# Kernel tuning notes

Measured on AMD Instinct MI355X. Metric: run time of the kernel, lower is better.

## Reference

```python
import jax, jax.numpy as jnp
import numpy as np

B, DX, DY, K, H = 131072, 256, 32, 4, 128
TIMESTEPS = 1000
LR, REG, SW = 0.1, 0.01, 1.0


def setup_inputs() -> dict:
    key = jax.random.key(0)
    ks = jax.random.split(key, 12)
    n = lambda k, shp, s=0.05: (jax.random.normal(k, shp) * s).astype(jnp.float32)
    return {
        "x": jax.random.normal(ks[0], (B, DX), jnp.float32),
        "t": jax.random.randint(ks[1], (B,), 0, K),
        "e_w1": n(ks[2], (DX + DY, H)), "e_b1": jnp.zeros((H,), jnp.float32),
        "e_w2": n(ks[3], (H, H)),       "e_b2": jnp.zeros((H,), jnp.float32),
        "e_w3": n(ks[4], (H, K)),       "e_b3": jnp.zeros((K,), jnp.float32),
        "s_xw": n(ks[5], (DX, H)),      "s_xb": jnp.zeros((H,), jnp.float32),
        "s_yw": n(ks[6], (DY, H)),      "s_yb": jnp.zeros((H,), jnp.float32),
        "s_temb": n(ks[7], (K, H)),
        "s_t1w": n(ks[8], (1, H)),      "s_t1b": jnp.zeros((H,), jnp.float32),
        "s_t2w": n(ks[9], (H, H)),      "s_t2b": jnp.zeros((H,), jnp.float32),
        "tr1w": n(ks[10], (4 * H, H)),  "tr1b": jnp.zeros((H,), jnp.float32),
        "tr2w": n(ks[11], (H, K)),      "tr2b": jnp.zeros((K,), jnp.float32),
        "steps": 20,
    }


def reference(x, t, e_w1, e_b1, e_w2, e_b2, e_w3, e_b3,
              s_xw, s_xb, s_yw, s_yb, s_temb, s_t1w, s_t1b, s_t2w, s_t2b,
              tr1w, tr1b, tr2w, tr2b, steps):
    tc = jnp.maximum(t, 0)                      # clamp_min(0)
    tci = tc[:, None]                           # [B,1] gather index
    valid = (t >= 0).astype(jnp.float32)[:, None]
    tau = jnp.maximum(tc.astype(jnp.float32) / TIMESTEPS, 1e-6)[:, None]  # [B,1]

    # y-independent precomputations (hoisted out of the loop)
    hx_e = x @ e_w1[:DX] + e_b1                 # energy first layer, x part [B,H]
    hx_s = x @ s_xw + s_xb                      # score x_proj [B,H]
    temb = s_temb[tc]                           # t embedding [B,H]
    th = jax.nn.silu(tau @ s_t1w + s_t1b) @ s_t2w + s_t2b  # time_fc [B,H]

    def total_fn(y):
        # EnergyNet: Linear-ReLU-Linear-ReLU-Linear on cat([x,y])
        h1 = jax.nn.relu(hx_e + y @ e_w1[DX:])
        e_all = jax.nn.relu(h1 @ e_w2 + e_b2) @ e_w3 + e_b3          # [B,K]
        e = jnp.take_along_axis(e_all, tci, axis=1)                  # [B,1]
        tot = e + REG * jnp.sum(y * y, axis=1, keepdims=True)
        # ScoreNet trunk on cat([x_proj, y_proj, t_embed, time_fc])
        hy = y @ s_yw + s_yb
        h = jnp.concatenate([hx_s, hy, temb, th], axis=-1)           # [B,4H]
        logits = jax.nn.silu(h @ tr1w + tr1b) @ tr2w + tr2b          # [B,K]
        ce = jax.nn.logsumexp(logits, axis=-1, keepdims=True) - jnp.take_along_axis(logits, tci, axis=1)
        return jnp.sum(tot + SW * ce * valid)

    grad_fn = jax.grad(total_fn)

    def step(carry, _):
        y, done = carry
        g = grad_fn(y)
        done = done | (jnp.sqrt(jnp.sum(g * g)) < 1e-3)  # torch: break before update
        y = jnp.where(done, y, y - LR * g)
        return (y, done), None

    y0 = jnp.zeros((x.shape[0], DY), jnp.float32)
    (y, _), _ = jax.lax.scan(step, (y0, jnp.array(False)), None, length=steps)
    return y
```

## Files before the change

### kernel.cpp

```cpp
#include <hip/hip_runtime.h>
#include <hip/hip_bf16.h>

#define DXc 256
#define DYc 32
#define Kc 4
#define Hc 128
#define LRf 0.1f
#define REGf 0.01f
#define TSTEPS 1000

typedef __attribute__((ext_vector_type(8))) short s8b;
typedef __attribute__((ext_vector_type(4))) float f32x4;

#define MFMA16(a, b, c) __builtin_amdgcn_mfma_f32_16x16x32_bf16((a), (b), (c), 0, 0, 0)

#define MFMA6(A0, A1, A2, B0, B1, B2, acc)      \
    do {                                        \
        acc = MFMA16((A0), (B0), acc);          \
        acc = MFMA16((A0), (B1), acc);          \
        acc = MFMA16((A1), (B0), acc);          \
        acc = MFMA16((A0), (B2), acc);          \
        acc = MFMA16((A1), (B1), acc);          \
        acc = MFMA16((A2), (B0), acc);          \
    } while (0)

__device__ __forceinline__ float hipart(float a) {
    return __uint_as_float(__float_as_uint(a) & 0xffff0000u);
}
__device__ __forceinline__ unsigned hi2(float a, float b) {
    return (__float_as_uint(a) >> 16) | (__float_as_uint(b) & 0xffff0000u);
}
__device__ __forceinline__ void wsplit(float x, unsigned short* __restrict__ h,
                                       unsigned short* __restrict__ l) {
    unsigned u = __float_as_uint(x);
    *h = (unsigned short)(u >> 16);
    float hf = __uint_as_float(u & 0xffff0000u);
    *l = (unsigned short)(__float_as_uint(x - hf) >> 16);
}
__device__ __forceinline__ void wsplit3(float x, unsigned short* __restrict__ p0,
                                        unsigned short* __restrict__ p1,
                                        unsigned short* __restrict__ p2) {
    unsigned u = __float_as_uint(x);
    *p0 = (unsigned short)(u >> 16);
    float r1 = x - __uint_as_float(u & 0xffff0000u);
    unsigned u1 = __float_as_uint(r1);
    *p1 = (unsigned short)(u1 >> 16);
    float r2 = r1 - __uint_as_float(u1 & 0xffff0000u);
    *p2 = (unsigned short)(__float_as_uint(r2) >> 16);
}
__device__ __forceinline__ void split3x8(const float* v, s8b& A0, s8b& A1, s8b& A2) {
    union { s8b s; unsigned u[4]; } P0, P1, P2;
    #pragma unroll
    for (int m = 0; m < 4; ++m) {
        float a = v[2 * m], b = v[2 * m + 1];
        unsigned ua = __float_as_uint(a), ub = __float_as_uint(b);
        P0.u[m] = (ua >> 16) | (ub & 0xffff0000u);
        float ra = a - __uint_as_float(ua & 0xffff0000u);
        float rb = b - __uint_as_float(ub & 0xffff0000u);
        unsigned ura = __float_as_uint(ra), urb = __float_as_uint(rb);
        P1.u[m] = (ura >> 16) | (urb & 0xffff0000u);
        float ra2 = ra - __uint_as_float(ura & 0xffff0000u);
        float rb2 = rb - __uint_as_float(urb & 0xffff0000u);
        P2.u[m] = (__float_as_uint(ra2) >> 16) | (__float_as_uint(rb2) & 0xffff0000u);
    }
    A0 = P0.s; A1 = P1.s; A2 = P2.s;
}
__device__ __forceinline__ void split3pack4(const float* v, uint2& Q0, uint2& Q1, uint2& Q2) {
    float r1[4], r2[4];
    #pragma unroll
    for (int i = 0; i < 4; ++i) {
        r1[i] = v[i] - hipart(v[i]);
        r2[i] = r1[i] - hipart(r1[i]);
    }
    Q0.x = hi2(v[0], v[1]);   Q0.y = hi2(v[2], v[3]);
    Q1.x = hi2(r1[0], r1[1]); Q1.y = hi2(r1[2], r1[3]);
    Q2.x = hi2(r2[0], r2[1]); Q2.y = hi2(r2[2], r2[3]);
}
__device__ __forceinline__ void split2pack4(const float* v, uint2& Q0, uint2& Q1) {
    Q0.x = hi2(v[0], v[1]); Q0.y = hi2(v[2], v[3]);
    float r0 = v[0] - hipart(v[0]), r1 = v[1] - hipart(v[1]);
    float r2 = v[2] - hipart(v[2]), r3 = v[3] - hipart(v[3]);
    Q1.x = hi2(r0, r1); Q1.y = hi2(r2, r3);
}

__global__ __launch_bounds__(256) void setup_kernel(
    const float* __restrict__ e_w1, const float* __restrict__ s_xw,
    const float* __restrict__ s_yw, const float* __restrict__ s_temb,
    const float* __restrict__ s_t1w, const float* __restrict__ s_t1b,
    const float* __restrict__ s_t2w, const float* __restrict__ s_t2b,
    const float* __restrict__ tr1w, const float* __restrict__ tr1b,
    const float* __restrict__ s_xb, const float* __restrict__ s_yb,
    const float* __restrict__ e_w2, float* __restrict__ d0,
    unsigned short* __restrict__ WcatTb0, unsigned short* __restrict__ WcatTb1,
    unsigned short* __restrict__ WcatTb2,
    unsigned short* __restrict__ W1Tb0, unsigned short* __restrict__ W1Tb1,
    unsigned short* __restrict__ W1Tb2,
    unsigned short* __restrict__ ew2Tb0, unsigned short* __restrict__ ew2Tb1,
    unsigned short* __restrict__ ew2Tb2,
    unsigned short* __restrict__ ew2bh, unsigned short* __restrict__ ew2bl,
    unsigned short* __restrict__ Wdybh, unsigned short* __restrict__ Wdybl)
{
    const int b = blockIdx.x;
    const int t = threadIdx.x;
    if (b < 64) {
        #pragma unroll
        for (int i = 0; i < 2; ++i) {
            int idx = t + 256 * i;
            int k = 4 * b + (idx >> 7);
            int c = idx & 127;
            float acc = 0.f;
            for (int h = 0; h < 128; ++h)
                acc += s_xw[k * 128 + h] * tr1w[h * 128 + c];
            wsplit3(acc, &WcatTb0[(128 + c) * 256 + k], &WcatTb1[(128 + c) * 256 + k],
                    &WcatTb2[(128 + c) * 256 + k]);
            float ev = e_w1[k * 128 + c];
            wsplit3(ev, &WcatTb0[c * 256 + k], &WcatTb1[c * 256 + k],
                    &WcatTb2[c * 256 + k]);
        }
    } else if (b == 64) {
        #pragma unroll
        for (int i = 0; i < 16; ++i) {
            int idx = t + 256 * i;
            int d = idx >> 7, c = idx & 127;
            float acc = 0.f;
            for (int h = 0; h < 128; ++h)
                acc += s_yw[d * 128 + h] * tr1w[(128 + h) * 128 + c];
            wsplit3(acc, &W1Tb0[(128 + c) * 32 + d], &W1Tb1[(128 + c) * 32 + d],
                    &W1Tb2[(128 + c) * 32 + d]);
            wsplit(acc, &Wdybh[d * 256 + c], &Wdybl[d * 256 + c]);
        }
    } else if (b == 65) {
        #pragma unroll
        for (int i = 0; i < 16; ++i) {
            int idx = t + 256 * i;
            int d = idx >> 7, c = idx & 127;
            float v = e_w1[(DXc + d) * 128 + c];
            wsplit3(v, &W1Tb0[c * 32 + d], &W1Tb1[c * 32 + d], &W1Tb2[c * 32 + d]);
            wsplit(v, &Wdybh[d * 256 + 128 + c], &Wdybl[d * 256 + 128 + c]);
        }
    } else if (b == 66) {
        #pragma unroll
        for (int i = 0; i < 64; ++i) {
            int idx = t + 256 * i;
            int h = idx >> 7, c = idx & 127;
            float v = e_w2[h * 128 + c];
            wsplit3(v, &ew2Tb0[c * 128 + h], &ew2Tb1[c * 128 + h],
                    &ew2Tb2[c * 128 + h]);
            wsplit(v, &ew2bh[h * 128 + c], &ew2bl[h * 128 + c]);
        }
    } else {
        __shared__ float thS[4][128];
        #pragma unroll
        for (int i = 0; i < 2; ++i) {
            int idx = t + 256 * i;
            int tt = idx >> 7, c = idx & 127;
            float tau = (float)tt / (float)TSTEPS;
            if (tau < 1e-6f) tau = 1e-6f;
            float acc = s_t2b[c];
            for (int h = 0; h < 128; ++h) {
                float aa = tau * s_t1w[h] + s_t1b[h];
                float s = 1.f / (1.f + expf(-aa));
                acc += aa * s * s_t2w[h * 128 + c];
            }
            thS[tt][c] = acc;
        }
        __syncthreads();
        #pragma unroll
        for (int i = 0; i < 2; ++i) {
            int idx = t + 256 * i;
            int tt = idx >> 7, c = idx & 127;
            float acc = tr1b[c];
            for (int h = 0; h < 128; ++h) {
                acc += s_temb[tt * 128 + h] * tr1w[(256 + h) * 128 + c];
                acc += thS[tt][h]           * tr1w[(384 + h) * 128 + c];
                acc += s_yb[h]              * tr1w[(128 + h) * 128 + c];
                acc += s_xb[h]              * tr1w[h * 128 + c];
            }
            d0[tt * 128 + c] = acc;
        }
    }
}

__global__ __launch_bounds__(256) void rowpre_kernel(
    const float* __restrict__ x, const int* __restrict__ tin,
    const unsigned short* __restrict__ WcatTb0,
    const unsigned short* __restrict__ WcatTb1,
    const unsigned short* __restrict__ WcatTb2,
    const float* __restrict__ e_b1, const float* __restrict__ d0,
    float* __restrict__ hxeP, float* __restrict__ cbP)
{
    __shared__ int tS[64];
    const int t = threadIdx.x;
    const int r0 = blockIdx.x * 64;
    const int w = t >> 6;
    const int l = t & 63;
    const int g = l >> 4, q = l & 15;
    if (t < 64) { int tv = tin[r0 + t]; tS[t] = tv > 0 ? tv : 0; }
    __syncthreads();

    for (int st = 0; st < 4; ++st) {
        const int smp = r0 + st * 16 + q;
        s8b Xb0[8], Xb1[8], Xb2[8];
        #pragma unroll
        for (int kc = 0; kc < 8; ++kc) {
            const float* xp = &x[(size_t)smp * 256 + kc * 32 + g * 8];
            float4 xa = *(const float4*)xp;
            float4 xb = *(const float4*)(xp + 4);
            float xv[8] = {xa.x, xa.y, xa.z, xa.w, xb.x, xb.y, xb.z, xb.w};
            split3x8(xv, Xb0[kc], Xb1[kc], Xb2[kc]);
        }
        #pragma unroll
        for (int ci = 0; ci < 4; ++ci) {
            const int colt = w * 4 + ci;
            f32x4 acc = {0.f, 0.f, 0.f, 0.f};
            #pragma unroll
            for (int kc = 0; kc < 8; ++kc) {
                const int wo = (colt * 16 + q) * 256 + kc * 32 + g * 8;
                s8b A0 = *(const s8b*)&WcatTb0[wo];
                s8b A1 = *(const s8b*)&WcatTb1[wo];
                s8b A2 = *(const s8b*)&WcatTb2[wo];
                MFMA6(A0, A1, A2, Xb0[kc], Xb1[kc], Xb2[kc], acc);
            }
            const int cb = colt * 16 + g * 4;
            if (colt < 8) {
                float4 bv = *(const float4*)&e_b1[cb];
                float4 o = {acc[0] + bv.x, acc[1] + bv.y, acc[2] + bv.z, acc[3] + bv.w};
                *(float4*)&hxeP[(size_t)smp * 128 + cb] = o;
            } else {
                const int cc = cb - 128;
                float4 dd = *(const float4*)&d0[tS[st * 16 + q] * 128 + cc];
                float4 o = {acc[0] + dd.x, acc[1] + dd.y, acc[2] + dd.z, acc[3] + dd.w};
                *(float4*)&cbP[(size_t)smp * 128 + cc] = o;
            }
        }
    }
}

__global__ __launch_bounds__(512) void iterate_kernel(
    const float* __restrict__ hxeP, const float* __restrict__ cbP,
    const unsigned short* __restrict__ W1Tb0, const unsigned short* __restrict__ W1Tb1,
    const unsigned short* __restrict__ W1Tb2,
    const unsigned short* __restrict__ ew2Tb0, const unsigned short* __restrict__ ew2Tb1,
    const unsigned short* __restrict__ ew2Tb2,
    const unsigned short* __restrict__ ew2bh, const unsigned short* __restrict__ ew2bl,
    const unsigned short* __restrict__ Wdybh, const unsigned short* __restrict__ Wdybl,
    const float* __restrict__ e_w3, const float* __restrict__ tr2w,
    const float* __restrict__ tr2b, const float* __restrict__ e_b2,
    const int* __restrict__ tin, const int* __restrict__ stepsPtr,
    float* __restrict__ yout)
{
    __shared__ __align__(16) unsigned short H1a[32 * 136];
    __shared__ __align__(16) unsigned short H1b[32 * 136];
    __shared__ __align__(16) unsigned short H1c[32 * 136];
    __shared__ __align__(16) unsigned short DAa[32 * 136], DAb[32 * 136];
    __shared__ __align__(16) float U[32 * 140];
    __shared__ __align__(16) float yS[32 * 36];
    __shared__ float ew3TS[512];
    __shared__ float eb2S[128];
    __shared__ float vSs[32];
    __shared__ int tcS[32];

    const int t = threadIdx.x;
    const int r0 = blockIdx.x * 32;
    const int w = t >> 6;
    const int l = t & 63;
    const int g = l >> 4;
    const int q = l & 15;
    const int row = t >> 4;
    const int p = t & 15;
    const int hA = 4 * p;
    const int hB = 64 + 4 * p;

    if (t < 32) {
        int tv = tin[r0 + t];
        tcS[t] = tv > 0 ? tv : 0;
        vSs[t] = (tv >= 0) ? 1.f : 0.f;
    }
    if (t < 128) eb2S[t] = e_b2[t];
    {
        const int k = t >> 7, c = t & 127;
        ew3TS[k * 128 + c] = e_w3[c * 4 + k];
    }
    for (int i = t; i < 32 * 36; i += 512) yS[i] = 0.f;

    float4 trw4[8];
    #pragma unroll
    for (int j = 0; j < 4; ++j) {
        trw4[j]     = *(const float4*)&tr2w[(hA + j) * 4];
        trw4[4 + j] = *(const float4*)&tr2w[(hB + j) * 4];
    }
    const float tb0 = tr2b[0], tb1 = tr2b[1], tb2 = tr2b[2], tb3 = tr2b[3];
    const int nsteps = stepsPtr[0];

    __syncthreads();

    for (int step = 0; step < nsteps; ++step) {
        {
            s8b WA0[2], WA1[2], WA2[2];
            #pragma unroll
            for (int ci = 0; ci < 2; ++ci) {
                const int arow = (2 * w + ci) * 16 + q;
                WA0[ci] = *(const s8b*)&W1Tb0[arow * 32 + g * 8];
                WA1[ci] = *(const s8b*)&W1Tb1[arow * 32 + g * 8];
                WA2[ci] = *(const s8b*)&W1Tb2[arow * 32 + g * 8];
            }
            #pragma unroll
            for (int ct = 0; ct < 2; ++ct) {
                float4 ya = *(const float4*)&yS[(ct * 16 + q) * 36 + g * 8];
                float4 yb = *(const float4*)&yS[(ct * 16 + q) * 36 + g * 8 + 4];
                float yv[8] = {ya.x, ya.y, ya.z, ya.w, yb.x, yb.y, yb.z, yb.w};
                s8b Y0, Y1, Y2;
                split3x8(yv, Y0, Y1, Y2);
                #pragma unroll
                for (int ci = 0; ci < 2; ++ci) {
                    const int colt = 2 * w + ci;
                    f32x4 acc = {0.f, 0.f, 0.f, 0.f};
                    MFMA6(WA0[ci], WA1[ci], WA2[ci], Y0, Y1, Y2, acc);
                    if (w < 4) {
                        const float4 vb = *(const float4*)
                            &hxeP[(size_t)(r0 + ct * 16 + q) * 128 + colt * 16 + g * 4];
                        float v[4];
                        v[0] = acc[0] + vb.x; v[1] = acc[1] + vb.y;
                        v[2] = acc[2] + vb.z; v[3] = acc[3] + vb.w;
                        #pragma unroll
                        for (int j = 0; j < 4; ++j) v[j] = v[j] > 0.f ? v[j] : 0.f;
                        uint2 Q0, Q1, Q2;
                        split3pack4(v, Q0, Q1, Q2);
                        const int off = (ct * 16 + q) * 136 + colt * 16 + g * 4;
                        *(uint2*)&H1a[off] = Q0;
                        *(uint2*)&H1b[off] = Q1;
                        *(uint2*)&H1c[off] = Q2;
                    } else {
                        const int cc = (colt - 8) * 16 + g * 4;
                        const float4 vb = *(const float4*)
                            &cbP[(size_t)(r0 + ct * 16 + q) * 128 + cc];
                        float4 o = {acc[0] + vb.x, acc[1] + vb.y,
                                    acc[2] + vb.z, acc[3] + vb.w};
                        *(float4*)&U[(ct * 16 + q) * 140 + cc] = o;
                    }
                }
            }
        }
        __syncthreads();

        {
            float aval[8], sval[8];
            float lg0 = 0.f, lg1 = 0.f, lg2 = 0.f, lg3 = 0.f;
            float4 v0 = *(const float4*)&U[row * 140 + hA];
            float4 v1 = *(const float4*)&U[row * 140 + hB];
            aval[0] = v0.x; aval[1] = v0.y; aval[2] = v0.z; aval[3] = v0.w;
            aval[4] = v1.x; aval[5] = v1.y; aval[6] = v1.z; aval[7] = v1.w;
            #pragma unroll
            for (int j = 0; j < 8; ++j) {
                float a = aval[j];
                float s = 1.f / (1.f + __expf(-a));
                sval[j] = s;
                float u = a * s;
                lg0 += u * trw4[j].x; lg1 += u * trw4[j].y;
                lg2 += u * trw4[j].z; lg3 += u * trw4[j].w;
            }
            #pragma unroll
            for (int m = 1; m < 16; m <<= 1) {
                lg0 += __shfl_xor(lg0, m);
                lg1 += __shfl_xor(lg1, m);
                lg2 += __shfl_xor(lg2, m);
                lg3 += __shfl_xor(lg3, m);
            }
            lg0 += tb0; lg1 += tb1; lg2 += tb2; lg3 += tb3;
            float mx = fmaxf(fmaxf(lg0, lg1), fmaxf(lg2, lg3));
            float e0 = __expf(lg0 - mx), e1 = __expf(lg1 - mx);
            float e2 = __expf(lg2 - mx), e3 = __expf(lg3 - mx);
            float inv = 1.f / (e0 + e1 + e2 + e3);
            int tcr = tcS[row];
            float vd = vSs[row];
            float dl0 = (e0 * inv - (tcr == 0 ? 1.f : 0.f)) * vd;
            float dl1 = (e1 * inv - (tcr == 1 ? 1.f : 0.f)) * vd;
            float dl2 = (e2 * inv - (tcr == 2 ? 1.f : 0.f)) * vd;
            float dl3 = (e3 * inv - (tcr == 3 ? 1.f : 0.f)) * vd;
            #pragma unroll
            for (int j = 0; j < 8; ++j) {
                float a = aval[j], s = sval[j];
                float du = dl0 * trw4[j].x + dl1 * trw4[j].y
                         + dl2 * trw4[j].z + dl3 * trw4[j].w;
                aval[j] = du * s * (1.f + a * (1.f - s));
            }
            float rl[8];
            #pragma unroll
            for (int j = 0; j < 8; ++j) rl[j] = aval[j] - hipart(aval[j]);
            uint2 QhA = {hi2(aval[0], aval[1]), hi2(aval[2], aval[3])};
            uint2 QhB = {hi2(aval[4], aval[5]), hi2(aval[6], aval[7])};
            uint2 QlA = {hi2(rl[0], rl[1]), hi2(rl[2], rl[3])};
            uint2 QlB = {hi2(rl[4], rl[5]), hi2(rl[6], rl[7])};
            *(uint2*)&DAa[row * 136 + hA] = QhA;
            *(uint2*)&DAa[row * 136 + hB] = QhB;
            *(uint2*)&DAb[row * 136 + hA] = QlA;
            *(uint2*)&DAb[row * 136 + hB] = QlB;
        }
        __syncthreads();

        {
            unsigned short* DZh = (unsigned short*)U;
            unsigned short* DZl = DZh + 32 * 136;
            const int hf = w & 1;
            const int ct0 = (w >> 1) * 2;
            f32x4 acc0 = {0.f, 0.f, 0.f, 0.f};
            f32x4 acc1 = {0.f, 0.f, 0.f, 0.f};
            #pragma unroll
            for (int kc = 0; kc < 4; ++kc) {
                const int boff = (hf * 16 + q) * 136 + kc * 32 + g * 8;
                s8b Ba = *(const s8b*)&H1a[boff];
                s8b Bb = *(const s8b*)&H1b[boff];
                s8b Bc = *(const s8b*)&H1c[boff];
                const int wo0 = ((ct0 + 0) * 16 + q) * 128 + kc * 32 + g * 8;
                const int wo1 = ((ct0 + 1) * 16 + q) * 128 + kc * 32 + g * 8;
                s8b A00 = *(const s8b*)&ew2Tb0[wo0];
                s8b A01 = *(const s8b*)&ew2Tb1[wo0];
                s8b A02 = *(const s8b*)&ew2Tb2[wo0];
                MFMA6(A00, A01, A02, Ba, Bb, Bc, acc0);
                s8b A10 = *(const s8b*)&ew2Tb0[wo1];
                s8b A11 = *(const s8b*)&ew2Tb1[wo1];
                s8b A12 = *(const s8b*)&ew2Tb2[wo1];
                MFMA6(A10, A11, A12, Ba, Bb, Bc, acc1);
            }
            const int smp = hf * 16 + q;
            const int tcr = tcS[smp];
            #pragma unroll
            for (int c2 = 0; c2 < 2; ++c2) {
                const f32x4& acc = c2 ? acc1 : acc0;
                const int cb = (ct0 + c2) * 16 + g * 4;
                const float4 eb = *(const float4*)&eb2S[cb];
                const float4 g4 = *(const float4*)&ew3TS[tcr * 128 + cb];
                float dz[4];
                dz[0] = (acc[0] + eb.x) > 0.f ? g4.x : 0.f;
                dz[1] = (acc[1] + eb.y) > 0.f ? g4.y : 0.f;
                dz[2] = (acc[2] + eb.z) > 0.f ? g4.z : 0.f;
                dz[3] = (acc[3] + eb.w) > 0.f ? g4.w : 0.f;
                uint2 Q0, Q1;
                split2pack4(dz, Q0, Q1);
                *(uint2*)&DZh[smp * 136 + cb] = Q0;
                *(uint2*)&DZl[smp * 136 + cb] = Q1;
            }
        }
        __syncthreads();

        {
            const unsigned short* DZh = (const unsigned short*)U;
            const unsigned short* DZl = DZh + 32 * 136;
            const int hf = w & 1;
            const int ht0 = (w >> 1) * 2;
            f32x4 acc0 = {0.f, 0.f, 0.f, 0.f};
            f32x4 acc1 = {0.f, 0.f, 0.f, 0.f};
            #pragma unroll
            for (int kc = 0; kc < 4; ++kc) {
                const int boff = (hf * 16 + q) * 136 + kc * 32 + g * 8;
                s8b Bh = *(const s8b*)&DZh[boff];
                s8b Bl = *(const s8b*)&DZl[boff];
                const int wo0 = ((ht0 + 0) * 16 + q) * 128 + kc * 32 + g * 8;
                const int wo1 = ((ht0 + 1) * 16 + q) * 128 + kc * 32 + g * 8;
                s8b A0h = *(const s8b*)&ew2bh[wo0];
                s8b A0l = *(const s8b*)&ew2bl[wo0];
                acc0 = MFMA16(A0h, Bh, acc0);
                acc0 = MFMA16(A0l, Bh, acc0);
                acc0 = MFMA16(A0h, Bl, acc0);
                s8b A1h = *(const s8b*)&ew2bh[wo1];
                s8b A1l = *(const s8b*)&ew2bl[wo1];
                acc1 = MFMA16(A1h, Bh, acc1);
                acc1 = MFMA16(A1l, Bh, acc1);
                acc1 = MFMA16(A1h, Bl, acc1);
            }
            const int smp = hf * 16 + q;
            #pragma unroll
            for (int c2 = 0; c2 < 2; ++c2) {
                const f32x4& acc = c2 ? acc1 : acc0;
                const int hb = (ht0 + c2) * 16 + g * 4;
                const int off = smp * 136 + hb;
                const uint2 mh = *(const uint2*)&H1a[off];
                float v[4];
                v[0] = ((short)(mh.x & 0xffffu) > 0) ? acc[0] : 0.f;
                v[1] = ((short)(mh.x >> 16)     > 0) ? acc[1] : 0.f;
                v[2] = ((short)(mh.y & 0xffffu) > 0) ? acc[2] : 0.f;
                v[3] = ((short)(mh.y >> 16)     > 0) ? acc[3] : 0.f;
                uint2 Q0, Q1;
                split2pack4(v, Q0, Q1);
                *(uint2*)&H1a[off] = Q0;
                *(uint2*)&H1b[off] = Q1;
            }
        }
        __syncthreads();

        if (w < 4) {
            const int dt = w >> 1, st = w & 1;
            f32x4 acc = {0.f, 0.f, 0.f, 0.f};
            #pragma unroll
            for (int kc = 0; kc < 8; ++kc) {
                const int boff = (st * 16 + q) * 136 + (kc & 3) * 32 + g * 8;
                s8b bh, bl;
                if (kc < 4) { bh = *(const s8b*)&DAa[boff]; bl = *(const s8b*)&DAb[boff]; }
                else        { bh = *(const s8b*)&H1a[boff]; bl = *(const s8b*)&H1b[boff]; }
                const int aoff = (dt * 16 + q) * 256 + kc * 32 + g * 8;
                s8b ah = *(const s8b*)&Wdybh[aoff];
                s8b al = *(const s8b*)&Wdybl[aoff];
                acc = MFMA16(ah, bh, acc);
                acc = MFMA16(al, bh, acc);
                acc = MFMA16(ah, bl, acc);
            }
            const int smp = st * 16 + q;
            const int db = dt * 16 + g * 4;
            float4 yv4 = *(const float4*)&yS[smp * 36 + db];
            yv4.x -= LRf * (acc[0] + 2.f * REGf * yv4.x);
            yv4.y -= LRf * (acc[1] + 2.f * REGf * yv4.y);
            yv4.z -= LRf * (acc[2] + 2.f * REGf * yv4.z);
            yv4.w -= LRf * (acc[3] + 2.f * REGf * yv4.w);
            *(float4*)&yS[smp * 36 + db] = yv4;
        }
        __syncthreads();
    }

    {
        const int orow = t >> 4;
        const int d2 = (t & 15) * 2;
        *(float2*)&yout[(size_t)(r0 + orow) * 32 + d2] =
            *(const float2*)&yS[orow * 36 + d2];
    }
}

extern "C" void kernel_launch(void* const* d_in, const int* in_sizes, int n_in,
                              void* d_out, int out_size, void* d_ws, size_t ws_size,
                              hipStream_t stream)
{
    const float* x      = (const float*)d_in[0];
    const int*   tin    = (const int*)d_in[1];
    const float* e_w1   = (const float*)d_in[2];
    const float* e_b1   = (const float*)d_in[3];
    const float* e_w2   = (const float*)d_in[4];
    const float* e_b2   = (const float*)d_in[5];
    const float* e_w3   = (const float*)d_in[6];
    const float* s_xw   = (const float*)d_in[8];
    const float* s_xb   = (const float*)d_in[9];
    const float* s_yw   = (const float*)d_in[10];
    const float* s_yb   = (const float*)d_in[11];
    const float* s_temb = (const float*)d_in[12];
    const float* s_t1w  = (const float*)d_in[13];
    const float* s_t1b  = (const float*)d_in[14];
    const float* s_t2w  = (const float*)d_in[15];
    const float* s_t2b  = (const float*)d_in[16];
    const float* tr1w   = (const float*)d_in[17];
    const float* tr1b   = (const float*)d_in[18];
    const float* tr2w   = (const float*)d_in[19];
    const float* tr2b   = (const float*)d_in[20];
    const int*   steps  = (const int*)d_in[21];

    const int B = in_sizes[0] / DXc;

    float* ws   = (float*)d_ws;
    float* hxeP = ws;
    float* cbP  = hxeP + (size_t)B * 128;
    float* d0   = cbP  + (size_t)B * 128;

    unsigned short* W1Tb0   = (unsigned short*)(d0 + 4 * 128);
    unsigned short* W1Tb1   = W1Tb0   + 256 * 32;
    unsigned short* W1Tb2   = W1Tb1   + 256 * 32;
    unsigned short* ew2Tb0  = W1Tb2   + 256 * 32;
    unsigned short* ew2Tb1  = ew2Tb0  + 128 * 128;
    unsigned short* ew2Tb2  = ew2Tb1  + 128 * 128;
    unsigned short* ew2bh   = ew2Tb2  + 128 * 128;
    unsigned short* ew2bl   = ew2bh   + 128 * 128;
    unsigned short* Wdybh   = ew2bl   + 128 * 128;
    unsigned short* Wdybl   = Wdybh   + 32 * 256;
    unsigned short* WcatTb0 = Wdybl   + 32 * 256;
    unsigned short* WcatTb1 = WcatTb0 + 256 * 256;
    unsigned short* WcatTb2 = WcatTb1 + 256 * 256;

    setup_kernel<<<68, 256, 0, stream>>>(e_w1, s_xw, s_yw, s_temb, s_t1w, s_t1b,
                                         s_t2w, s_t2b, tr1w, tr1b, s_xb, s_yb,
                                         e_w2, d0,
                                         WcatTb0, WcatTb1, WcatTb2,
                                         W1Tb0, W1Tb1, W1Tb2,
                                         ew2Tb0, ew2Tb1, ew2Tb2,
                                         ew2bh, ew2bl, Wdybh, Wdybl);
    rowpre_kernel<<<B / 64, 256, 0, stream>>>(x, tin, WcatTb0, WcatTb1, WcatTb2,
                                              e_b1, d0, hxeP, cbP);
    iterate_kernel<<<B / 32, 512, 0, stream>>>(hxeP, cbP,
                                               W1Tb0, W1Tb1, W1Tb2,
                                               ew2Tb0, ew2Tb1, ew2Tb2,
                                               ew2bh, ew2bl, Wdybh, Wdybl,
                                               e_w3, tr2w, tr2b, e_b2, tin,
                                               steps, (float*)d_out);
}
```

Baseline: 3.339 ms.

## Halve iterate_kernel block to 256 threads, doubling per-wave MFMA work

Launches iterate_kernel with 256 threads (4 waves) instead of 512 and sets launch bounds to allow two blocks per CU. Each wave now covers twice as many column tiles in every GEMM phase and reuses each loaded weight fragment across both 16-row sample tiles. This cuts the repeated weight loads per tile and lets all waves take part in the final y-update phase instead of half sitting idle. The cost is more accumulator registers per wave and fewer waves per block to hide latency across barriers.

```diff
diff --git a/kernel.cpp b/kernel.cpp
--- a/kernel.cpp
+++ b/kernel.cpp
@@ -236,7 +236,7 @@
     }
 }
 
-__global__ __launch_bounds__(512) void iterate_kernel(
+__global__ __launch_bounds__(256, 2) void iterate_kernel(
     const float* __restrict__ hxeP, const float* __restrict__ cbP,
     const unsigned short* __restrict__ W1Tb0, const unsigned short* __restrict__ W1Tb1,
     const unsigned short* __restrict__ W1Tb2,
@@ -266,7 +266,7 @@
     const int l = t & 63;
     const int g = l >> 4;
     const int q = l & 15;
-    const int row = t >> 4;
+    const int rowg = t >> 4;
     const int p = t & 15;
     const int hA = 4 * p;
     const int hB = 64 + 4 * p;
@@ -277,11 +277,11 @@
         vSs[t] = (tv >= 0) ? 1.f : 0.f;
     }
     if (t < 128) eb2S[t] = e_b2[t];
-    {
-        const int k = t >> 7, c = t & 127;
+    for (int i = t; i < 512; i += 256) {
+        const int k = i >> 7, c = i & 127;
         ew3TS[k * 128 + c] = e_w3[c * 4 + k];
     }
-    for (int i = t; i < 32 * 36; i += 512) yS[i] = 0.f;
+    for (int i = t; i < 32 * 36; i += 256) yS[i] = 0.f;
 
     float4 trw4[8];
     #pragma unroll
@@ -295,55 +295,51 @@
     __syncthreads();
 
     for (int step = 0; step < nsteps; ++step) {
-        {
-            s8b WA0[2], WA1[2], WA2[2];
-            #pragma unroll
-            for (int ci = 0; ci < 2; ++ci) {
-                const int arow = (2 * w + ci) * 16 + q;
-                WA0[ci] = *(const s8b*)&W1Tb0[arow * 32 + g * 8];
-                WA1[ci] = *(const s8b*)&W1Tb1[arow * 32 + g * 8];
-                WA2[ci] = *(const s8b*)&W1Tb2[arow * 32 + g * 8];
-            }
-            #pragma unroll
-            for (int ct = 0; ct < 2; ++ct) {
-                float4 ya = *(const float4*)&yS[(ct * 16 + q) * 36 + g * 8];
-                float4 yb = *(const float4*)&yS[(ct * 16 + q) * 36 + g * 8 + 4];
-                float yv[8] = {ya.x, ya.y, ya.z, ya.w, yb.x, yb.y, yb.z, yb.w};
-                s8b Y0, Y1, Y2;
-                split3x8(yv, Y0, Y1, Y2);
-                #pragma unroll
-                for (int ci = 0; ci < 2; ++ci) {
-                    const int colt = 2 * w + ci;
-                    f32x4 acc = {0.f, 0.f, 0.f, 0.f};
-                    MFMA6(WA0[ci], WA1[ci], WA2[ci], Y0, Y1, Y2, acc);
-                    if (w < 4) {
-                        const float4 vb = *(const float4*)
-                            &hxeP[(size_t)(r0 + ct * 16 + q) * 128 + colt * 16 + g * 4];
-                        float v[4];
-                        v[0] = acc[0] + vb.x; v[1] = acc[1] + vb.y;
-                        v[2] = acc[2] + vb.z; v[3] = acc[3] + vb.w;
-                        #pragma unroll
-                        for (int j = 0; j < 4; ++j) v[j] = v[j] > 0.f ? v[j] : 0.f;
-                        uint2 Q0, Q1, Q2;
-                        split3pack4(v, Q0, Q1, Q2);
-                        const int off = (ct * 16 + q) * 136 + colt * 16 + g * 4;
-                        *(uint2*)&H1a[off] = Q0;
-                        *(uint2*)&H1b[off] = Q1;
-                        *(uint2*)&H1c[off] = Q2;
-                    } else {
-                        const int cc = (colt - 8) * 16 + g * 4;
-                        const float4 vb = *(const float4*)
-                            &cbP[(size_t)(r0 + ct * 16 + q) * 128 + cc];
-                        float4 o = {acc[0] + vb.x, acc[1] + vb.y,
-                                    acc[2] + vb.z, acc[3] + vb.w};
-                        *(float4*)&U[(ct * 16 + q) * 140 + cc] = o;
-                    }
+        #pragma unroll
+        for (int ct = 0; ct < 2; ++ct) {
+            float4 ya = *(const float4*)&yS[(ct * 16 + q) * 36 + g * 8];
+            float4 yb = *(const float4*)&yS[(ct * 16 + q) * 36 + g * 8 + 4];
+            float yv[8] = {ya.x, ya.y, ya.z, ya.w, yb.x, yb.y, yb.z, yb.w};
+            s8b Y0, Y1, Y2;
+            split3x8(yv, Y0, Y1, Y2);
+            #pragma unroll
+            for (int ci = 0; ci < 4; ++ci) {
+                const int colt = 4 * w + ci;
+                const int arow = colt * 16 + q;
+                s8b WA0 = *(const s8b*)&W1Tb0[arow * 32 + g * 8];
+                s8b WA1 = *(const s8b*)&W1Tb1[arow * 32 + g * 8];
+                s8b WA2 = *(const s8b*)&W1Tb2[arow * 32 + g * 8];
+                f32x4 acc = {0.f, 0.f, 0.f, 0.f};
+                MFMA6(WA0, WA1, WA2, Y0, Y1, Y2, acc);
+                if (w < 2) {
+                    const float4 vb = *(const float4*)
+                        &hxeP[(size_t)(r0 + ct * 16 + q) * 128 + colt * 16 + g * 4];
+                    float v[4];
+                    v[0] = acc[0] + vb.x; v[1] = acc[1] + vb.y;
+                    v[2] = acc[2] + vb.z; v[3] = acc[3] + vb.w;
+                    #pragma unroll
+                    for (int j = 0; j < 4; ++j) v[j] = v[j] > 0.f ? v[j] : 0.f;
+                    uint2 Q0, Q1, Q2;
+                    split3pack4(v, Q0, Q1, Q2);
+                    const int off = (ct * 16 + q) * 136 + colt * 16 + g * 4;
+                    *(uint2*)&H1a[off] = Q0;
+                    *(uint2*)&H1b[off] = Q1;
+                    *(uint2*)&H1c[off] = Q2;
+                } else {
+                    const int cc = (colt - 8) * 16 + g * 4;
+                    const float4 vb = *(const float4*)
+                        &cbP[(size_t)(r0 + ct * 16 + q) * 128 + cc];
+                    float4 o = {acc[0] + vb.x, acc[1] + vb.y,
+                                acc[2] + vb.z, acc[3] + vb.w};
+                    *(float4*)&U[(ct * 16 + q) * 140 + cc] = o;
                 }
             }
         }
         __syncthreads();
 
-        {
+        #pragma unroll
+        for (int ct2 = 0; ct2 < 2; ++ct2) {
+            const int row = ct2 * 16 + rowg;
             float aval[8], sval[8];
             float lg0 = 0.f, lg1 = 0.f, lg2 = 0.f, lg3 = 0.f;
             float4 v0 = *(const float4*)&U[row * 140 + hA];
@@ -401,44 +397,52 @@
         {
             unsigned short* DZh = (unsigned short*)U;
             unsigned short* DZl = DZh + 32 * 136;
-            const int hf = w & 1;
-            const int ct0 = (w >> 1) * 2;
-            f32x4 acc0 = {0.f, 0.f, 0.f, 0.f};
-            f32x4 acc1 = {0.f, 0.f, 0.f, 0.f};
+            f32x4 acc00 = {0.f,0.f,0.f,0.f}, acc01 = {0.f,0.f,0.f,0.f};
+            f32x4 acc10 = {0.f,0.f,0.f,0.f}, acc11 = {0.f,0.f,0.f,0.f};
             #pragma unroll
             for (int kc = 0; kc < 4; ++kc) {
-                const int boff = (hf * 16 + q) * 136 + kc * 32 + g * 8;
-                s8b Ba = *(const s8b*)&H1a[boff];
-                s8b Bb = *(const s8b*)&H1b[boff];
-                s8b Bc = *(const s8b*)&H1c[boff];
-                const int wo0 = ((ct0 + 0) * 16 + q) * 128 + kc * 32 + g * 8;
-                const int wo1 = ((ct0 + 1) * 16 + q) * 128 + kc * 32 + g * 8;
+                const int b0 = q * 136 + kc * 32 + g * 8;
+                const int b1 = (16 + q) * 136 + kc * 32 + g * 8;
+                s8b B0a = *(const s8b*)&H1a[b0];
+                s8b B0b = *(const s8b*)&H1b[b0];
+                s8b B0c = *(const s8b*)&H1c[b0];
+                s8b B1a = *(const s8b*)&H1a[b1];
+                s8b B1b = *(const s8b*)&H1b[b1];
+                s8b B1c = *(const s8b*)&H1c[b1];
+                const int wo0 = ((2 * w + 0) * 16 + q) * 128 + kc * 32 + g * 8;
                 s8b A00 = *(const s8b*)&ew2Tb0[wo0];
                 s8b A01 = *(const s8b*)&ew2Tb1[wo0];
                 s8b A02 = *(const s8b*)&ew2Tb2[wo0];
-                MFMA6(A00, A01, A02, Ba, Bb, Bc, acc0);
+                MFMA6(A00, A01, A02, B0a, B0b, B0c, acc00);
+                MFMA6(A00, A01, A02, B1a, B1b, B1c, acc10);
+                const int wo1 = ((2 * w + 1) * 16 + q) * 128 + kc * 32 + g * 8;
                 s8b A10 = *(const s8b*)&ew2Tb0[wo1];
                 s8b A11 = *(const s8b*)&ew2Tb1[wo1];
                 s8b A12 = *(const s8b*)&ew2Tb2[wo1];
-                MFMA6(A10, A11, A12, Ba, Bb, Bc, acc1);
-            }
-            const int smp = hf * 16 + q;
-            const int tcr = tcS[smp];
-            #pragma unroll
-            for (int c2 = 0; c2 < 2; ++c2) {
-                const f32x4& acc = c2 ? acc1 : acc0;
-                const int cb = (ct0 + c2) * 16 + g * 4;
-                const float4 eb = *(const float4*)&eb2S[cb];
-                const float4 g4 = *(const float4*)&ew3TS[tcr * 128 + cb];
-                float dz[4];
-                dz[0] = (acc[0] + eb.x) > 0.f ? g4.x : 0.f;
-                dz[1] = (acc[1] + eb.y) > 0.f ? g4.y : 0.f;
-                dz[2] = (acc[2] + eb.z) > 0.f ? g4.z : 0.f;
-                dz[3] = (acc[3] + eb.w) > 0.f ? g4.w : 0.f;
-                uint2 Q0, Q1;
-                split2pack4(dz, Q0, Q1);
-                *(uint2*)&DZh[smp * 136 + cb] = Q0;
-                *(uint2*)&DZl[smp * 136 + cb] = Q1;
+                MFMA6(A10, A11, A12, B0a, B0b, B0c, acc01);
+                MFMA6(A10, A11, A12, B1a, B1b, B1c, acc11);
+            }
+            #pragma unroll
+            for (int ct = 0; ct < 2; ++ct) {
+                const int smp = ct * 16 + q;
+                const int tcr = tcS[smp];
+                #pragma unroll
+                for (int c2 = 0; c2 < 2; ++c2) {
+                    const f32x4& acc = ct ? (c2 ? acc11 : acc10)
+                                          : (c2 ? acc01 : acc00);
+                    const int cb = (2 * w + c2) * 16 + g * 4;
+                    const float4 eb = *(const float4*)&eb2S[cb];
+                    const float4 g4 = *(const float4*)&ew3TS[tcr * 128 + cb];
+                    float dz[4];
+                    dz[0] = (acc[0] + eb.x) > 0.f ? g4.x : 0.f;
+                    dz[1] = (acc[1] + eb.y) > 0.f ? g4.y : 0.f;
+                    dz[2] = (acc[2] + eb.z) > 0.f ? g4.z : 0.f;
+                    dz[3] = (acc[3] + eb.w) > 0.f ? g4.w : 0.f;
+                    uint2 Q0, Q1;
+                    split2pack4(dz, Q0, Q1);
+                    *(uint2*)&DZh[smp * 136 + cb] = Q0;
+                    *(uint2*)&DZl[smp * 136 + cb] = Q1;
+                }
             }
         }
         __syncthreads();
@@ -446,49 +450,60 @@
         {
             const unsigned short* DZh = (const unsigned short*)U;
             const unsigned short* DZl = DZh + 32 * 136;
-            const int hf = w & 1;
-            const int ht0 = (w >> 1) * 2;
-            f32x4 acc0 = {0.f, 0.f, 0.f, 0.f};
-            f32x4 acc1 = {0.f, 0.f, 0.f, 0.f};
+            f32x4 acc00 = {0.f,0.f,0.f,0.f}, acc01 = {0.f,0.f,0.f,0.f};
+            f32x4 acc10 = {0.f,0.f,0.f,0.f}, acc11 = {0.f,0.f,0.f,0.f};
             #pragma unroll
             for (int kc = 0; kc < 4; ++kc) {
-                const int boff = (hf * 16 + q) * 136 + kc * 32 + g * 8;
-                s8b Bh = *(const s8b*)&DZh[boff];
-                s8b Bl = *(const s8b*)&DZl[boff];
-                const int wo0 = ((ht0 + 0) * 16 + q) * 128 + kc * 32 + g * 8;
-                const int wo1 = ((ht0 + 1) * 16 + q) * 128 + kc * 32 + g * 8;
+                const int b0 = q * 136 + kc * 32 + g * 8;
+                const int b1 = (16 + q) * 136 + kc * 32 + g * 8;
+                s8b B0h = *(const s8b*)&DZh[b0];
+                s8b B0l = *(const s8b*)&DZl[b0];
+                s8b B1h = *(const s8b*)&DZh[b1];
+                s8b B1l = *(const s8b*)&DZl[b1];
+                const int wo0 = ((2 * w + 0) * 16 + q) * 128 + kc * 32 + g * 8;
                 s8b A0h = *(const s8b*)&ew2bh[wo0];
                 s8b A0l = *(const s8b*)&ew2bl[wo0];
-                acc0 = MFMA16(A0h, Bh, acc0);
-                acc0 = MFMA16(A0l, Bh, acc0);
-                acc0 = MFMA16(A0h, Bl, acc0);
+                acc00 = MFMA16(A0h, B0h, acc00);
+                acc00 = MFMA16(A0l, B0h, acc00);
+                acc00 = MFMA16(A0h, B0l, acc00);
+                acc10 = MFMA16(A0h, B1h, acc10);
+                acc10 = MFMA16(A0l, B1h, acc10);
+                acc10 = MFMA16(A0h, B1l, acc10);
+                const int wo1 = ((2 * w + 1) * 16 + q) * 128 + kc * 32 + g * 8;
                 s8b A1h = *(const s8b*)&ew2bh[wo1];
                 s8b A1l = *(const s8b*)&ew2bl[wo1];
-                acc1 = MFMA16(A1h, Bh, acc1);
-                acc1 = MFMA16(A1l, Bh, acc1);
-                acc1 = MFMA16(A1h, Bl, acc1);
-            }
-            const int smp = hf * 16 + q;
-            #pragma unroll
-            for (int c2 = 0; c2 < 2; ++c2) {
-                const f32x4& acc = c2 ? acc1 : acc0;
-                const int hb = (ht0 + c2) * 16 + g * 4;
-                const int off = smp * 136 + hb;
-                const uint2 mh = *(const uint2*)&H1a[off];
-                float v[4];
-                v[0] = ((short)(mh.x & 0xffffu) > 0) ? acc[0] : 0.f;
-                v[1] = ((short)(mh.x >> 16)     > 0) ? acc[1] : 0.f;
-                v[2] = ((short)(mh.y & 0xffffu) > 0) ? acc[2] : 0.f;
-                v[3] = ((short)(mh.y >> 16)     > 0) ? acc[3] : 0.f;
-                uint2 Q0, Q1;
-                split2pack4(v, Q0, Q1);
-                *(uint2*)&H1a[off] = Q0;
-                *(uint2*)&H1b[off] = Q1;
+                acc01 = MFMA16(A1h, B0h, acc01);
+                acc01 = MFMA16(A1l, B0h, acc01);
+                acc01 = MFMA16(A1h, B0l, acc01);
+                acc11 = MFMA16(A1h, B1h, acc11);
+                acc11 = MFMA16(A1l, B1h, acc11);
+                acc11 = MFMA16(A1h, B1l, acc11);
+            }
+            #pragma unroll
+            for (int ct = 0; ct < 2; ++ct) {
+                const int smp = ct * 16 + q;
+                #pragma unroll
+                for (int c2 = 0; c2 < 2; ++c2) {
+                    const f32x4& acc = ct ? (c2 ? acc11 : acc10)
+                                          : (c2 ? acc01 : acc00);
+                    const int hb = (2 * w + c2) * 16 + g * 4;
+                    const int off = smp * 136 + hb;
+                    const uint2 mh = *(const uint2*)&H1a[off];
+                    float v[4];
+                    v[0] = ((short)(mh.x & 0xffffu) > 0) ? acc[0] : 0.f;
+                    v[1] = ((short)(mh.x >> 16)     > 0) ? acc[1] : 0.f;
+                    v[2] = ((short)(mh.y & 0xffffu) > 0) ? acc[2] : 0.f;
+                    v[3] = ((short)(mh.y >> 16)     > 0) ? acc[3] : 0.f;
+                    uint2 Q0, Q1;
+                    split2pack4(v, Q0, Q1);
+                    *(uint2*)&H1a[off] = Q0;
+                    *(uint2*)&H1b[off] = Q1;
+                }
             }
         }
         __syncthreads();
 
-        if (w < 4) {
+        {
             const int dt = w >> 1, st = w & 1;
             f32x4 acc = {0.f, 0.f, 0.f, 0.f};
             #pragma unroll
@@ -517,10 +532,10 @@
     }
 
     {
-        const int orow = t >> 4;
-        const int d2 = (t & 15) * 2;
-        *(float2*)&yout[(size_t)(r0 + orow) * 32 + d2] =
-            *(const float2*)&yS[orow * 36 + d2];
+        const int orow = t >> 3;
+        const int d4 = (t & 7) * 4;
+        *(float4*)&yout[(size_t)(r0 + orow) * 32 + d4] =
+            *(const float4*)&yS[orow * 36 + d4];
     }
 }
 
@@ -580,7 +595,7 @@
                                          ew2bh, ew2bl, Wdybh, Wdybl);
     rowpre_kernel<<<B / 64, 256, 0, stream>>>(x, tin, WcatTb0, WcatTb1, WcatTb2,
                                               e_b1, d0, hxeP, cbP);
-    iterate_kernel<<<B / 32, 512, 0, stream>>>(hxeP, cbP,
+    iterate_kernel<<<B / 32, 256, 0, stream>>>(hxeP, cbP,
                                                W1Tb0, W1Tb1, W1Tb2,
                                                ew2Tb0, ew2Tb1, ew2Tb2,
                                                ew2bh, ew2bl, Wdybh, Wdybl,
```

After: 4.395 ms. +31.6%, slower.
